# Optimization experiments

Hardware: AMD Instinct MI355X
Metric: run time of the kernel (lower is better)

## Reference

```python
import jax, jax.numpy as jnp
import numpy as np

L = 12; D = 768; H = 12; HD = 64; FF = 3072; P = 16; IMG = 224; BLK = 64
LORA = 16.0 / 64.0  # lora_alpha / r
PD = 512; B = 8


def _ln(x, g, b, eps=1e-6):
    m = x.mean(-1, keepdims=True)
    v = ((x - m) ** 2).mean(-1, keepdims=True)
    return (x - m) * jax.lax.rsqrt(v + eps) * g + b


def _dq(q, s):
    # int4 codes [O, I] + blockwise absmax-style scales [O, I//BLK] -> fp32 weight
    O, I = q.shape
    return ((q.astype(jnp.float32).reshape(O, I // BLK, BLK) - 7.5) * s[:, :, None]).reshape(O, I)


def _forward(img, patch_w, patch_b, cls_token, ln1_g, ln1_b, ln2_g, ln2_b, g1, g2,
             qkv_s, qkv_b, a_qkv, b_qkv, proj_s, proj_b, a_proj, b_proj,
             fc1_s, fc1_b, fc2_s, fc2_b, fcn_g, fcn_b, head_w, head_b,
             qkv_q, proj_q, fc1_q, fc2_q):
    x = img[:, 0]                                   # [B,3,224,224]
    Bn = x.shape[0]
    gp = IMG // P
    # patch embed (conv16x16/s16 == unfold + matmul)
    p = x.reshape(Bn, 3, gp, P, gp, P).transpose(0, 2, 4, 1, 3, 5).reshape(Bn, gp * gp, 3 * P * P)
    tok = p @ patch_w.T + patch_b                   # [B,196,768]
    cls = jnp.broadcast_to(cls_token, (Bn, 1, D))
    x = jnp.concatenate([cls, tok], axis=1)         # [B,197,768]

    def block(x, pr):
        (l1g, l1b, l2g, l2b, gm1, gm2, qq, qs, qb, aQ, bQ,
         pq, ps, pb, aP, bP, f1q, f1s, f1b, f2q, f2s, f2b) = pr
        h = _ln(x, l1g, l1b)
        # fused dequant + matmul + LoRA (qkv)
        qkv = h @ _dq(qq, qs).T + qb + LORA * ((h @ aQ.T) @ bQ.T)  # [B,N,3D]
        q, k, v = jnp.split(qkv, 3, axis=-1)
        heads = lambda t: t.reshape(Bn, -1, H, HD).transpose(0, 2, 1, 3)
        q, k, v = heads(q), heads(k), heads(v)
        attn = jax.nn.softmax(jnp.einsum('bhnd,bhmd->bhnm', q, k) / np.sqrt(HD).astype(np.float32), axis=-1)
        o = jnp.einsum('bhnm,bhmd->bhnd', attn, v).transpose(0, 2, 1, 3).reshape(Bn, -1, D)
        # dequant + matmul + LoRA (attn out proj)
        o = o @ _dq(pq, ps).T + pb + LORA * ((o @ aP.T) @ bP.T)
        x = x + gm1 * o                             # layerscale residual
        h = _ln(x, l2g, l2b)
        h = jax.nn.gelu(h @ _dq(f1q, f1s).T + f1b)
        h = h @ _dq(f2q, f2s).T + f2b
        x = x + gm2 * h
        return x, None

    xs = (ln1_g, ln1_b, ln2_g, ln2_b, g1, g2, qkv_q, qkv_s, qkv_b, a_qkv, b_qkv,
          proj_q, proj_s, proj_b, a_proj, b_proj, fc1_q, fc1_s, fc1_b, fc2_q, fc2_s, fc2_b)
    x, _ = jax.lax.scan(block, x, xs)
    pooled = x[:, 1:].mean(axis=1)                  # BEiT avg-pool over patch tokens
    pooled = _ln(pooled, fcn_g, fcn_b)              # fc_norm
    return jax.nn.relu(pooled @ head_w.T + head_b)  # Linear + ReLU projection -> [B,512]


def setup_inputs() -> dict:
    key = jax.random.key(0)
    ks = jax.random.split(key, 24)
    f = lambda i, sh, sc=0.02: jax.random.normal(ks[i], sh, dtype=jnp.float32) * sc
    u = lambda i, sh: jax.random.uniform(ks[i], sh, dtype=jnp.float32) * 0.01 + 1e-3
    qi = lambda i, sh: jax.random.randint(ks[i], sh, 0, 16, dtype=jnp.int32)
    return {
        'img': f(0, (B, 1, 3, IMG, IMG), 1.0),
        'patch_w': f(1, (D, 3 * P * P)), 'patch_b': jnp.zeros((D,), jnp.float32),
        'cls_token': f(2, (1, 1, D)),
        'ln1_g': jnp.ones((L, D), jnp.float32), 'ln1_b': jnp.zeros((L, D), jnp.float32),
        'ln2_g': jnp.ones((L, D), jnp.float32), 'ln2_b': jnp.zeros((L, D), jnp.float32),
        'g1': jnp.full((L, D), 0.1, jnp.float32), 'g2': jnp.full((L, D), 0.1, jnp.float32),
        'qkv_q': qi(3, (L, 3 * D, D)), 'qkv_s': u(4, (L, 3 * D, D // BLK)), 'qkv_b': f(5, (L, 3 * D)),
        'a_qkv': f(6, (L, 64, D)), 'b_qkv': f(7, (L, 3 * D, 64)),
        'proj_q': qi(8, (L, D, D)), 'proj_s': u(9, (L, D, D // BLK)), 'proj_b': jnp.zeros((L, D), jnp.float32),
        'a_proj': f(10, (L, 64, D)), 'b_proj': f(11, (L, D, 64)),
        'fc1_q': qi(12, (L, FF, D)), 'fc1_s': u(13, (L, FF, D // BLK)), 'fc1_b': jnp.zeros((L, FF), jnp.float32),
        'fc2_q': qi(14, (L, D, FF)), 'fc2_s': u(15, (L, D, FF // BLK)), 'fc2_b': jnp.zeros((L, D), jnp.float32),
        'fcn_g': jnp.ones((D,), jnp.float32), 'fcn_b': jnp.zeros((D,), jnp.float32),
        'head_w': f(16, (PD, D)), 'head_b': jnp.zeros((PD,), jnp.float32),
    }


def reference(img, patch_w, patch_b, cls_token, ln1_g, ln1_b, ln2_g, ln2_b, g1, g2,
              qkv_q, qkv_s, qkv_b, a_qkv, b_qkv, proj_q, proj_s, proj_b, a_proj, b_proj,
              fc1_q, fc1_s, fc1_b, fc2_q, fc2_s, fc2_b, fcn_g, fcn_b, head_w, head_b):
    return _forward(img, patch_w, patch_b, cls_token, ln1_g, ln1_b, ln2_g, ln2_b, g1, g2,
                    qkv_s, qkv_b, a_qkv, b_qkv, proj_s, proj_b, a_proj, b_proj,
                    fc1_s, fc1_b, fc2_s, fc2_b, fcn_g, fcn_b, head_w, head_b,
                    qkv_q, proj_q, fc1_q, fc2_q)
```

## Files before the change

kernel.cpp:

```cpp
#include <hip/hip_runtime.h>
#include <hip/hip_bf16.h>

using bf16 = __hip_bfloat16;
typedef __attribute__((ext_vector_type(8))) short short8;
typedef __attribute__((ext_vector_type(4))) float f32x4;
typedef __attribute__((ext_vector_type(4))) int i32x4;

#define NTOK 197
#define MTOK 1576
#define MPATCH 1568

static __device__ __forceinline__ float bf2f(bf16 v){ return __bfloat162float(v); }
static __device__ __forceinline__ bf16 f2bf(float v){ return __float2bfloat16(v); }
static __device__ __forceinline__ unsigned pk2(float a, float b){
  union{ bf16 h[2]; unsigned u; } r; r.h[0]=f2bf(a); r.h[1]=f2bf(b); return r.u;
}

static __device__ __forceinline__ float gelu_tanh(float x){
  float x3 = x*x*x;
  float a = 0.7978845608028654f*(x + 0.044715f*x3);
  float e = __expf(-2.f*fabsf(a));
  float t = (1.f-e)/(1.f+e);
  t = (a >= 0.f) ? t : -t;
  return 0.5f*x*(1.f+t);
}

static __device__ __forceinline__ void gload16(const void* g, void* l){
  __builtin_amdgcn_global_load_lds(
      (const __attribute__((address_space(1))) unsigned*)g,
      (__attribute__((address_space(3))) unsigned*)l, 16, 0, 0);
}

template<int N> static __device__ __forceinline__ void wait_vm(){
  if constexpr (N==3)      asm volatile("s_waitcnt vmcnt(3)" ::: "memory");
  else if constexpr (N==5) asm volatile("s_waitcnt vmcnt(5)" ::: "memory");
  else                     asm volatile("s_waitcnt vmcnt(0)" ::: "memory");
}

template<int K>
static __device__ __forceinline__ void dq16(const int* __restrict__ q,
                                            const float* __restrict__ s,
                                            bf16* __restrict__ o, int j){
  constexpr int KP16 = K/16;
  int n = j / KP16;
  int k = (j - n*KP16) * 16;
  const i32x4* qp = (const i32x4*)(q + (size_t)n*K + k);
  i32x4 a0 = __builtin_nontemporal_load(qp);
  i32x4 a1 = __builtin_nontemporal_load(qp + 1);
  i32x4 a2 = __builtin_nontemporal_load(qp + 2);
  i32x4 a3 = __builtin_nontemporal_load(qp + 3);
  float sc = s[(size_t)n*(K>>6) + (k>>6)];
  uint4 r0, r1;
  r0.x = pk2(((float)a0.x-7.5f)*sc, ((float)a0.y-7.5f)*sc);
  r0.y = pk2(((float)a0.z-7.5f)*sc, ((float)a0.w-7.5f)*sc);
  r0.z = pk2(((float)a1.x-7.5f)*sc, ((float)a1.y-7.5f)*sc);
  r0.w = pk2(((float)a1.z-7.5f)*sc, ((float)a1.w-7.5f)*sc);
  r1.x = pk2(((float)a2.x-7.5f)*sc, ((float)a2.y-7.5f)*sc);
  r1.y = pk2(((float)a2.z-7.5f)*sc, ((float)a2.w-7.5f)*sc);
  r1.z = pk2(((float)a3.x-7.5f)*sc, ((float)a3.y-7.5f)*sc);
  r1.w = pk2(((float)a3.z-7.5f)*sc, ((float)a3.w-7.5f)*sc);
  bf16* op = o + (size_t)n*K + k;
  *(uint4*)(op)     = r0;
  *(uint4*)(op + 8) = r1;
}

template<int K>
__global__ void dq_k(const int* __restrict__ q, const float* __restrict__ s,
                     bf16* __restrict__ o, int total16){
  #pragma unroll 2
  for (int j = blockIdx.x*256 + threadIdx.x; j < total16; j += gridDim.x*256)
    dq16<K>(q, s, o, j);
}

__global__ void cvtall_k(const float* __restrict__ patchw, bf16* __restrict__ patchwb,
                         const float* __restrict__ headw, bf16* __restrict__ headwb,
                         const float* __restrict__ bQ, bf16* __restrict__ bQs,
                         const float* __restrict__ bP, bf16* __restrict__ bPs){
  const int R0 = 768*768/4, R1 = R0 + 512*768/4;
  const int R2 = R1 + 12*2304*64/4, R3 = R2 + 12*768*64/4;
  for (int i = blockIdx.x*256 + threadIdx.x; i < R3; i += gridDim.x*256){
    const float* in; bf16* out; float a; int j;
    if (i < R0){ in=patchw; out=patchwb; a=1.f; j=i; }
    else if (i < R1){ in=headw; out=headwb; a=1.f; j=i-R0; }
    else if (i < R2){ in=bQ; out=bQs; a=0.25f; j=i-R1; }
    else { in=bP; out=bPs; a=0.25f; j=i-R2; }
    float4 v = *(const float4*)(in + (size_t)j*4);
    uint2 r; r.x = pk2(v.x*a, v.y*a); r.y = pk2(v.z*a, v.w*a);
    *(uint2*)(out + (size_t)j*4) = r;
  }
}

__global__ __launch_bounds__(256) void transall_k(const float* __restrict__ aQ, bf16* __restrict__ aQT,
                                                  const float* __restrict__ aP, bf16* __restrict__ aPT){
  __shared__ float tile[64][65];
  const float* in = blockIdx.z ? aP : aQ;
  bf16* out = blockIdx.z ? aPT : aQT;
  const int l = blockIdx.y, c0 = blockIdx.x*64;
  const int t = threadIdx.x;
  const int r = t >> 2, cq = (t & 3) * 16;
  const float* src = in + (size_t)l*64*768 + (size_t)r*768 + c0 + cq;
  #pragma unroll
  for (int j=0;j<4;j++){
    float4 v = *(const float4*)(src + j*4);
    tile[r][cq + j*4 + 0] = v.x; tile[r][cq + j*4 + 1] = v.y;
    tile[r][cq + j*4 + 2] = v.z; tile[r][cq + j*4 + 3] = v.w;
  }
  __syncthreads();
  unsigned w[8];
  #pragma unroll
  for (int j=0;j<8;j++)
    w[j] = pk2(tile[cq + 2*j][r], tile[cq + 2*j + 1][r]);
  bf16* dst = out + ((size_t)l*768 + c0 + r)*64 + cq;
  *(uint4*)(dst)     = *(uint4*)&w[0];
  *(uint4*)(dst + 8) = *(uint4*)&w[4];
}

__global__ void patchify_k(const float* __restrict__ img, bf16* __restrict__ p){
  int idx = blockIdx.x*256 + threadIdx.x;
  if (idx >= MPATCH*768) return;
  int col = idx % 768, pr = idx / 768;
  int b = pr / 196, patch = pr % 196;
  int c = col >> 8, rem = col & 255, py = rem >> 4, px = rem & 15;
  int gy = patch / 14, gx = patch % 14;
  float v = img[(((size_t)(b*3 + c))*224 + gy*16 + py)*224 + gx*16 + px];
  p[idx] = f2bf(v);
}

__global__ void cls_k(const float* __restrict__ cls, float* __restrict__ x){
  int i = blockIdx.x*256 + threadIdx.x;
  if (i >= 8*768) return;
  int b = i / 768, d = i % 768;
  x[(size_t)(b*NTOK)*768 + d] = cls[d];
}

__global__ __launch_bounds__(256) void ln_k(const float* __restrict__ x,
                                            const float* __restrict__ g,
                                            const float* __restrict__ b,
                                            bf16* __restrict__ out, int M){
  int row = blockIdx.x*4 + (threadIdx.x >> 6);
  int lane = threadIdx.x & 63;
  if (row >= M) return;
  const float* xr = x + (size_t)row*768;
  float4 v[3]; float s = 0.f;
  #pragma unroll
  for (int j=0;j<3;j++){
    v[j] = *(const float4*)(xr + lane*4 + j*256);
    s += v[j].x + v[j].y + v[j].z + v[j].w;
  }
  #pragma unroll
  for (int o=32;o;o>>=1) s += __shfl_xor(s, o);
  float mean = s * (1.f/768.f);
  float vs = 0.f;
  #pragma unroll
  for (int j=0;j<3;j++){
    float dx=v[j].x-mean, dy=v[j].y-mean, dz=v[j].z-mean, dw=v[j].w-mean;
    vs += dx*dx + dy*dy + dz*dz + dw*dw;
  }
  #pragma unroll
  for (int o=32;o;o>>=1) vs += __shfl_xor(vs, o);
  float rs = rsqrtf(vs*(1.f/768.f) + 1e-6f);
  bf16* orow = out + (size_t)row*768;
  #pragma unroll
  for (int j=0;j<3;j++){
    int d0 = lane*4 + j*256;
    float4 gv = *(const float4*)(g + d0);
    float4 bv = *(const float4*)(b + d0);
    uint2 pk;
    pk.x = pk2((v[j].x-mean)*rs*gv.x + bv.x, (v[j].y-mean)*rs*gv.y + bv.y);
    pk.y = pk2((v[j].z-mean)*rs*gv.z + bv.z, (v[j].w-mean)*rs*gv.w + bv.w);
    *(uint2*)(orow + d0) = pk;
  }
}

__global__ __launch_bounds__(256) void attn_k(const bf16* __restrict__ qkv, bf16* __restrict__ o){
  __shared__ char Kc[2][32*128];
  __shared__ bf16 Vt[2][64][40];
  __shared__ bf16 Pl[4][32][40];

  const int blk = blockIdx.x;
  const int half = blk & 1, bh = blk >> 1;
  const int b = bh / 12, h = bh % 12;
  const int t = threadIdx.x, wave = t>>6, lane = t&63;
  const int qbase = half*128 + wave*32;
  const bf16* base = qkv + (size_t)b*NTOK*2304 + h*64;

  short8 qf[2][2];
  #pragma unroll
  for (int qt=0;qt<2;qt++){
    int row = qbase + qt*16 + (lane&15); row = row < NTOK ? row : NTOK-1;
    const bf16* qr = base + (size_t)row*2304 + (lane>>4)*8;
    qf[qt][0] = *(const short8*)(qr);
    qf[qt][1] = *(const short8*)(qr + 32);
  }

  f32x4 Oa[2][4];
  float mrow[2][4], srow[2][4];
  #pragma unroll
  for (int i=0;i<2;i++)
    #pragma unroll
    for (int j=0;j<4;j++){ Oa[i][j] = (f32x4){0.f,0.f,0.f,0.f}; }
  #pragma unroll
  for (int i=0;i<2;i++)
    #pragma unroll
    for (int j=0;j<4;j++){ mrow[i][j] = -1e30f; srow[i][j] = 0.f; }

  const int sr = t>>3, sc = (t&7)*8;
  auto ldK = [&](int c)->uint4{
    int kv = c*32 + sr; kv = kv < NTOK ? kv : NTOK-1;
    return *(const uint4*)(base + (size_t)kv*2304 + 768 + sc);
  };
  auto ldV = [&](int c)->uint4{
    int kv = c*32 + sr;
    uint4 r = {0,0,0,0};
    if (kv < NTOK) r = *(const uint4*)(base + (size_t)kv*2304 + 1536 + sc);
    return r;
  };
  auto wrK = [&](int buf, uint4 kvv){
    *(uint4*)(Kc[buf] + sr*128 + ((sc*2) ^ ((sr&7)<<4))) = kvv;
  };
  auto wrV = [&](int buf, uint4 vvv){
    union{ uint4 u; short s[8]; } w; w.u = vvv;
    #pragma unroll
    for (int j=0;j<8;j++) *(short*)&Vt[buf][sc+j][sr] = w.s[j];
  };

  { uint4 k0 = ldK(0), v0 = ldV(0); wrK(0,k0); wrV(0,v0); }
  __syncthreads();

  for (int c=0;c<7;c++){
    const int buf = c & 1;
    uint4 kn, vn; const bool pf = (c < 6);
    if (pf){ kn = ldK(c+1); vn = ldV(c+1); }

    f32x4 S[2][2];
    #pragma unroll
    for (int i=0;i<2;i++)
      #pragma unroll
      for (int j=0;j<2;j++) S[i][j] = (f32x4){0.f,0.f,0.f,0.f};
    #pragma unroll
    for (int kt=0;kt<2;kt++){
      int rk = kt*16 + (lane&15);
      const char* kb = Kc[buf] + rk*128;
      int swz = (rk&7)<<4;
      short8 b0 = *(const short8*)(kb + (((lane>>4)*16) ^ swz));
      short8 b1 = *(const short8*)(kb + ((64 + (lane>>4)*16) ^ swz));
      #pragma unroll
      for (int qt=0;qt<2;qt++){
        S[qt][kt] = __builtin_amdgcn_mfma_f32_16x16x32_bf16(qf[qt][0], b0, S[qt][kt],0,0,0);
        S[qt][kt] = __builtin_amdgcn_mfma_f32_16x16x32_bf16(qf[qt][1], b1, S[qt][kt],0,0,0);
      }
    }

    #pragma unroll
    for (int qt=0;qt<2;qt++){
      #pragma unroll
      for (int r=0;r<4;r++){
        float s0 = S[qt][0][r]*0.125f, s1 = S[qt][1][r]*0.125f;
        if (c == 6){
          if (192 + (lane&15) >= NTOK) s0 = -1e30f;
          s1 = -1e30f;
        }
        float mx = fmaxf(s0, s1);
        mx = fmaxf(mx, __shfl_xor(mx,1));
        mx = fmaxf(mx, __shfl_xor(mx,2));
        mx = fmaxf(mx, __shfl_xor(mx,4));
        mx = fmaxf(mx, __shfl_xor(mx,8));
        float mo = mrow[qt][r];
        float mn = fmaxf(mo, mx);
        float scl = __expf(mo - mn);
        mrow[qt][r] = mn;
        float p0 = __expf(s0 - mn), p1 = __expf(s1 - mn);
        srow[qt][r] = srow[qt][r]*scl + p0 + p1;
        #pragma unroll
        for (int dt=0;dt<4;dt++) Oa[qt][dt][r] *= scl;
        int pr = qt*16 + (lane>>4)*4 + r;
        Pl[wave][pr][lane&15]      = f2bf(p0);
        Pl[wave][pr][16+(lane&15)] = f2bf(p1);
      }
    }

    short8 vb[4];
    #pragma unroll
    for (int dt=0;dt<4;dt++)
      vb[dt] = *(const short8*)(&Vt[buf][dt*16+(lane&15)][(lane>>4)*8]);
    #pragma unroll
    for (int qt=0;qt<2;qt++){
      short8 pa = *(const short8*)(&Pl[wave][qt*16+(lane&15)][(lane>>4)*8]);
      #pragma unroll
      for (int dt=0;dt<4;dt++)
        Oa[qt][dt] = __builtin_amdgcn_mfma_f32_16x16x32_bf16(pa, vb[dt], Oa[qt][dt],0,0,0);
    }

    if (pf){ wrK(buf^1, kn); wrV(buf^1, vn); }
    __syncthreads();
  }

  #pragma unroll
  for (int qt=0;qt<2;qt++)
    #pragma unroll
    for (int r=0;r<4;r++){
      float s = srow[qt][r];
      s += __shfl_xor(s,1); s += __shfl_xor(s,2);
      s += __shfl_xor(s,4); s += __shfl_xor(s,8);
      srow[qt][r] = 1.f/s;
    }
  #pragma unroll
  for (int qt=0;qt<2;qt++){
    #pragma unroll
    for (int r=0;r<4;r++){
      int tok = qbase + qt*16 + (lane>>4)*4 + r;
      if (tok < NTOK){
        bf16* orow = o + ((size_t)(b*NTOK+tok))*768 + h*64 + (lane&15);
        float inv = srow[qt][r];
        #pragma unroll
        for (int dt=0;dt<4;dt++) orow[dt*16] = f2bf(Oa[qt][dt][r]*inv);
      }
    }
  }
}

__global__ void pool_k(const float* __restrict__ x, float* __restrict__ pooled){
  int idx = blockIdx.x*256 + threadIdx.x;
  if (idx >= 8*768) return;
  int b = idx / 768, d = idx % 768;
  const float* col = x + (size_t)(b*NTOK)*768 + d;
  float s0=0.f, s1=0.f, s2=0.f, s3=0.f;
  for (int i=1; i<=196; i+=4){
    s0 += col[(size_t)i*768];
    s1 += col[(size_t)(i+1)*768];
    s2 += col[(size_t)(i+2)*768];
    s3 += col[(size_t)(i+3)*768];
  }
  pooled[idx] = (s0+s1+s2+s3) * (1.f/196.f);
}

template<int BM, int BN, int OUTMODE, int ACT, int FOLD>
__global__ __launch_bounds__(256) void gemm_k(
    const bf16* __restrict__ A, const bf16* __restrict__ W,
    const float* __restrict__ bias, const float* __restrict__ gvec,
    void* __restrict__ Cout,
    int M, int N, int Kst, int kiters, size_t kslab)
{
  constexpr int WCM = BM/2;
  constexpr int WCN = BN/2;
  constexpr int FM  = WCM/16;
  constexpr int FN  = WCN/16;
  constexpr int NW  = BN/32;
  constexpr int LCNT = 1 + NW;

  __shared__ char As[2][BM*128];
  __shared__ char Bs[2][BN*128];

  int mt, nt;
  {
    int gmy = gridDim.y;
    int nwg = gridDim.x * gmy;
    int bid = blockIdx.y * gridDim.x + blockIdx.x;
    int q8 = nwg >> 3, r8 = nwg & 7, xcd = bid & 7, idx = bid >> 3;
    int swz = (xcd < r8 ? xcd*(q8+1) : r8*(q8+1) + (xcd-r8)*q8) + idx;
    nt = swz / gmy; mt = swz - nt*gmy;
  }
  if (FOLD){
    A += (size_t)blockIdx.z * (size_t)M * 64;
    W += (size_t)blockIdx.z * (size_t)N * 64;
  }
  const int kz = FOLD ? 0 : blockIdx.z;
  const int k0 = kz * kiters;
  const int t = threadIdx.x, wave = t>>6, lane = t&63;
  const int wr = wave>>1, wc = wave&1;
  const int KT = kiters;

  const int srow = t >> 3;
  const int swzc = ((t&7)<<4) ^ ((srow&7)<<4);

  f32x4 acc[FM][FN];
  #pragma unroll
  for (int i=0;i<FM;i++)
    #pragma unroll
    for (int j=0;j<FN;j++) acc[i][j] = (f32x4){0.f,0.f,0.f,0.f};

  auto STAGE = [&](int it, int buf){
    {
      int gm = mt*BM + srow; gm = gm < M ? gm : M-1;
      gload16((const char*)A + (size_t)gm*Kst*2 + (size_t)(k0+it)*128 + swzc,
              As[buf] + wave*1024);
    }
    #pragma unroll
    for (int c=0;c<NW;c++){
      int gn = nt*BN + 32*c + srow;
      gload16((const char*)W + (size_t)gn*Kst*2 + (size_t)(k0+it)*128 + swzc,
              Bs[buf] + c*4096 + wave*1024);
    }
  };

  const int lrow = lane & 15;
  const int lkb  = (lane >> 4) * 16;
  auto computeTile = [&](int buf){
    __builtin_amdgcn_s_setprio(1);
    #pragma unroll
    for (int kk=0; kk<2; kk++){
      short8 af[FM]; short8 bw[FN];
      #pragma unroll
      for (int f=0; f<FM; f++){
        int ra = wr*WCM + f*16 + lrow;
        af[f] = *(const short8*)(As[buf] + ra*128 + ((kk*64 + lkb) ^ ((ra&7)<<4)));
      }
      #pragma unroll
      for (int f=0; f<FN; f++){
        int rb = wc*WCN + f*16 + lrow;
        bw[f] = *(const short8*)(Bs[buf] + rb*128 + ((kk*64 + lkb) ^ ((rb&7)<<4)));
      }
      #pragma unroll
      for (int i=0;i<FM;i++)
        #pragma unroll
        for (int j=0;j<FN;j++)
          acc[i][j] = __builtin_amdgcn_mfma_f32_16x16x32_bf16(af[i], bw[j], acc[i][j], 0, 0, 0);
    }
    __builtin_amdgcn_s_setprio(0);
  };

  STAGE(0, 0);
  if (KT > 1) STAGE(1, 1);

  for (int it = 0; it < KT; ++it){
    if (it == KT-1) wait_vm<0>(); else wait_vm<LCNT>();
    __builtin_amdgcn_s_barrier();
    computeTile(it & 1);
    asm volatile("s_waitcnt lgkmcnt(0)" ::: "memory");
    __builtin_amdgcn_s_barrier();
    if (it+2 < KT) STAGE(it+2, it & 1);
  }

  const int erow = (lane >> 4) * 4, ecol = lane & 15;
  #pragma unroll
  for (int i=0;i<FM;i++){
    #pragma unroll
    for (int j=0;j<FN;j++){
      int n = nt*BN + wc*WCN + j*16 + ecol;
      float bv = (bias != nullptr) ? bias[n] : 0.f;
      float gv = (OUTMODE==2) ? gvec[n] : 0.f;
      #pragma unroll
      for (int q=0; q<4; q++){
        int m = mt*BM + wr*WCM + i*16 + erow + q;
        if (m < M){
          float v = acc[i][j][q] + bv;
          if (ACT == 1) v = gelu_tanh(v);
          if (ACT == 2) v = fmaxf(v, 0.f);
          size_t off = (size_t)m*N + n;
          if (OUTMODE == 0)      ((float*)Cout)[(size_t)kz*kslab + off] = v;
          else if (OUTMODE == 1) ((bf16*)Cout)[off] = f2bf(v);
          else if (OUTMODE == 2) ((float*)Cout)[off] += gv * v;
          else if (OUTMODE == 4){
            int bb = m / 196, rr = m - bb*196;
            ((float*)Cout)[((size_t)(bb*NTOK + rr + 1))*768 + n] = v;
          }
          else {
            bf16* C = (bf16*)Cout + (FOLD ? (size_t)blockIdx.z*(size_t)M*N : (size_t)0);
            C[off] = f2bf(bf2f(C[off]) + v);
          }
        }
      }
    }
  }
}

extern "C" void kernel_launch(void* const* d_in, const int* in_sizes, int n_in,
                              void* d_out, int out_size, void* d_ws, size_t ws_size,
                              hipStream_t stream){
  (void)in_sizes; (void)n_in; (void)out_size; (void)ws_size;
  const float* img    = (const float*)d_in[0];
  const float* patchw = (const float*)d_in[1];
  const float* patchb = (const float*)d_in[2];
  const float* cls    = (const float*)d_in[3];
  const float* ln1g   = (const float*)d_in[4];
  const float* ln1b   = (const float*)d_in[5];
  const float* ln2g   = (const float*)d_in[6];
  const float* ln2b   = (const float*)d_in[7];
  const float* g1     = (const float*)d_in[8];
  const float* g2     = (const float*)d_in[9];
  const int*   qkvq   = (const int*)d_in[10];
  const float* qkvs   = (const float*)d_in[11];
  const float* qkvb   = (const float*)d_in[12];
  const float* aQ     = (const float*)d_in[13];
  const float* bQ     = (const float*)d_in[14];
  const int*   projq  = (const int*)d_in[15];
  const float* projs  = (const float*)d_in[16];
  const float* projb  = (const float*)d_in[17];
  const float* aP     = (const float*)d_in[18];
  const float* bP     = (const float*)d_in[19];
  const int*   fc1q   = (const int*)d_in[20];
  const float* fc1s   = (const float*)d_in[21];
  const float* fc1b   = (const float*)d_in[22];
  const int*   fc2q   = (const int*)d_in[23];
  const float* fc2s   = (const float*)d_in[24];
  const float* fc2b   = (const float*)d_in[25];
  const float* fcn_g  = (const float*)d_in[26];
  const float* fcn_b  = (const float*)d_in[27];
  const float* headw  = (const float*)d_in[28];
  const float* headb  = (const float*)d_in[29];
  float* out = (float*)d_out;

  char* wp = (char*)d_ws;
  auto alloc = [&](size_t bytes)->char* {
    char* r = wp; wp += (bytes + 255) & ~(size_t)255; return r;
  };
  float* x      = (float*)alloc((size_t)MTOK*768*4);
  bf16*  qkvo   = (bf16*) alloc((size_t)MTOK*2304*2);
  bf16*  h      = (bf16*) alloc((size_t)MTOK*768*2);
  bf16*  h1     = (bf16*) alloc((size_t)MTOK*3072*2);
  bf16*  ob     = (bf16*) alloc((size_t)MTOK*768*2);
  bf16*  p      = (bf16*) alloc((size_t)MPATCH*768*2);
  float* pooled = (float*)alloc((size_t)8*768*4);
  bf16*  pooledb= (bf16*) alloc((size_t)8*768*2);
  bf16* wqb = (bf16*)alloc((size_t)12*2304*768*2);
  bf16* wpb = (bf16*)alloc((size_t)12*768*768*2);
  bf16* w1b = (bf16*)alloc((size_t)12*3072*768*2);
  bf16* w2b = (bf16*)alloc((size_t)12*768*3072*2);
  bf16* patchwb = (bf16*)alloc((size_t)768*768*2);
  bf16* headwb  = (bf16*)alloc((size_t)512*768*2);
  bf16* bQs = (bf16*)alloc((size_t)12*2304*64*2);
  bf16* bPs = (bf16*)alloc((size_t)12*768*64*2);
  bf16* aQT = (bf16*)alloc((size_t)12*768*64*2);
  bf16* aPT = (bf16*)alloc((size_t)12*768*64*2);

  const int GM32 = (MTOK + 31) / 32;

  dq_k<768><<<2048, 256, 0, stream>>>(qkvq, qkvs, wqb, 12*2304*768/16);
  dq_k<768><<<2048, 256, 0, stream>>>(projq, projs, wpb, 12*768*768/16);
  dq_k<768><<<2048, 256, 0, stream>>>(fc1q, fc1s, w1b, 6*3072*768/16);
  dq_k<768><<<2048, 256, 0, stream>>>(fc1q + (size_t)6*3072*768, fc1s + (size_t)6*3072*12,
                                      w1b + (size_t)6*3072*768, 6*3072*768/16);
  dq_k<3072><<<2048, 256, 0, stream>>>(fc2q, fc2s, w2b, 6*768*3072/16);
  dq_k<3072><<<2048, 256, 0, stream>>>(fc2q + (size_t)6*768*3072, fc2s + (size_t)6*768*48,
                                       w2b + (size_t)6*768*3072, 6*768*3072/16);
  cvtall_k<<<1024, 256, 0, stream>>>(patchw, patchwb, headw, headwb, bQ, bQs, bP, bPs);
  transall_k<<<dim3(12, 12, 2), 256, 0, stream>>>(aQ, aQT, aP, aPT);
  gemm_k<32,64,3,0,1><<<dim3(768/64, 2304/32, 12), 256, 0, stream>>>(
      bQs, aQT, nullptr, nullptr, wqb, 2304, 768, 64, 1, 0);
  gemm_k<32,64,3,0,1><<<dim3(768/64, 768/32, 12), 256, 0, stream>>>(
      bPs, aPT, nullptr, nullptr, wpb, 768, 768, 64, 1, 0);

  patchify_k<<<(MPATCH*768 + 255)/256, 256, 0, stream>>>(img, p);
  gemm_k<32,64,4,0,0><<<dim3(768/64, MPATCH/32, 1), 256, 0, stream>>>(
      p, patchwb, patchb, nullptr, x, MPATCH, 768, 768, 12, 0);
  cls_k<<<(8*768 + 255)/256, 256, 0, stream>>>(cls, x);

  for (int l=0; l<12; l++){
    const bf16* wq_l = wqb + (size_t)l*2304*768;
    const bf16* wp_l = wpb + (size_t)l*768*768;
    const bf16* w1_l = w1b + (size_t)l*3072*768;
    const bf16* w2_l = w2b + (size_t)l*768*3072;

    ln_k<<<(MTOK+3)/4, 256, 0, stream>>>(x, ln1g + l*768, ln1b + l*768, h, MTOK);
    gemm_k<32,128,1,0,0><<<dim3(2304/128, GM32, 1), 256, 0, stream>>>(
        h, wq_l, qkvb + (size_t)l*2304, nullptr, qkvo, MTOK, 2304, 768, 12, 0);
    attn_k<<<192, 256, 0, stream>>>(qkvo, ob);
    gemm_k<32,64,2,0,0><<<dim3(768/64, GM32, 1), 256, 0, stream>>>(
        ob, wp_l, projb + (size_t)l*768, g1 + l*768, x, MTOK, 768, 768, 12, 0);

    ln_k<<<(MTOK+3)/4, 256, 0, stream>>>(x, ln2g + l*768, ln2b + l*768, h, MTOK);
    gemm_k<32,128,1,1,0><<<dim3(3072/128, GM32, 1), 256, 0, stream>>>(
        h, w1_l, fc1b + (size_t)l*3072, nullptr, h1, MTOK, 3072, 768, 12, 0);
    gemm_k<32,64,2,0,0><<<dim3(768/64, GM32, 1), 256, 0, stream>>>(
        h1, w2_l, fc2b + (size_t)l*768, g2 + l*768, x, MTOK, 768, 3072, 48, 0);
  }

  pool_k<<<(8*768 + 255)/256, 256, 0, stream>>>(x, pooled);
  ln_k<<<2, 256, 0, stream>>>(pooled, fcn_g, fcn_b, pooledb, 8);
  gemm_k<32,128,0,2,0><<<dim3(512/128, 1, 1), 256, 0, stream>>>(
      pooledb, headwb, headb, nullptr, out, 8, 512, 768, 12, 0);
}
```

Baseline: 1.473 ms.

## Split attention into 64-query blocks and fuse pooling, norm and head

The attention kernel now uses 128-thread blocks with 4 query groups per batch-head, giving 384 blocks instead of 192. Waves whose queries fall past the sequence end skip compute but still help load K/V tiles. Separately, mean pooling, final layernorm and the head linear+ReLU are fused into one tail kernel, replacing three launches. The variance in the tail kernel is now computed as E[x^2]-mean^2, which can lose precision compared with the two-pass form.

After: 1.541 ms. 1.05x slower.

```diff
diff --git a/kernel.cpp b/kernel.cpp
--- a/kernel.cpp
+++ b/kernel.cpp
@@ -12,6 +12,9 @@
 
 static __device__ __forceinline__ float bf2f(bf16 v){ return __bfloat162float(v); }
 static __device__ __forceinline__ bf16 f2bf(float v){ return __float2bfloat16(v); }
+static __device__ __forceinline__ float bfs(short s){
+  union{ unsigned u; float f; } c; c.u = ((unsigned)(unsigned short)s) << 16; return c.f;
+}
 static __device__ __forceinline__ unsigned pk2(float a, float b){
   union{ bf16 h[2]; unsigned u; } r; r.h[0]=f2bf(a); r.h[1]=f2bf(b); return r.u;
 }
@@ -172,25 +175,28 @@
   }
 }
 
-__global__ __launch_bounds__(256) void attn_k(const bf16* __restrict__ qkv, bf16* __restrict__ o){
+__global__ __launch_bounds__(128) void attn_k(const bf16* __restrict__ qkv, bf16* __restrict__ o){
   __shared__ char Kc[2][32*128];
   __shared__ bf16 Vt[2][64][40];
-  __shared__ bf16 Pl[4][32][40];
+  __shared__ bf16 Pl[2][32][40];
 
   const int blk = blockIdx.x;
-  const int half = blk & 1, bh = blk >> 1;
+  const int grp = blk & 3, bh = blk >> 2;
   const int b = bh / 12, h = bh % 12;
   const int t = threadIdx.x, wave = t>>6, lane = t&63;
-  const int qbase = half*128 + wave*32;
+  const int qbase = grp*64 + wave*32;
+  const bool alive = qbase < NTOK;
   const bf16* base = qkv + (size_t)b*NTOK*2304 + h*64;
 
   short8 qf[2][2];
-  #pragma unroll
-  for (int qt=0;qt<2;qt++){
-    int row = qbase + qt*16 + (lane&15); row = row < NTOK ? row : NTOK-1;
-    const bf16* qr = base + (size_t)row*2304 + (lane>>4)*8;
-    qf[qt][0] = *(const short8*)(qr);
-    qf[qt][1] = *(const short8*)(qr + 32);
+  if (alive){
+    #pragma unroll
+    for (int qt=0;qt<2;qt++){
+      int row = qbase + qt*16 + (lane&15); row = row < NTOK ? row : NTOK-1;
+      const bf16* qr = base + (size_t)row*2304 + (lane>>4)*8;
+      qf[qt][0] = *(const short8*)(qr);
+      qf[qt][1] = *(const short8*)(qr + 32);
+    }
   }
 
   f32x4 Oa[2][4];
@@ -198,140 +204,192 @@
   #pragma unroll
   for (int i=0;i<2;i++)
     #pragma unroll
-    for (int j=0;j<4;j++){ Oa[i][j] = (f32x4){0.f,0.f,0.f,0.f}; }
-  #pragma unroll
-  for (int i=0;i<2;i++)
-    #pragma unroll
-    for (int j=0;j<4;j++){ mrow[i][j] = -1e30f; srow[i][j] = 0.f; }
-
-  const int sr = t>>3, sc = (t&7)*8;
-  auto ldK = [&](int c)->uint4{
+    for (int j=0;j<4;j++){ Oa[i][j] = (f32x4){0.f,0.f,0.f,0.f}; mrow[i][j] = -1e30f; srow[i][j] = 0.f; }
+
+  const int sr = t>>2, scq = (t&3)*16;
+  auto ldK = [&](int c, uint4& k0, uint4& k1){
     int kv = c*32 + sr; kv = kv < NTOK ? kv : NTOK-1;
-    return *(const uint4*)(base + (size_t)kv*2304 + 768 + sc);
+    const bf16* kp = base + (size_t)kv*2304 + 768 + scq;
+    k0 = *(const uint4*)(kp);
+    k1 = *(const uint4*)(kp + 8);
   };
-  auto ldV = [&](int c)->uint4{
+  auto ldV = [&](int c, uint4& v0, uint4& v1){
     int kv = c*32 + sr;
-    uint4 r = {0,0,0,0};
-    if (kv < NTOK) r = *(const uint4*)(base + (size_t)kv*2304 + 1536 + sc);
-    return r;
+    v0 = (uint4){0,0,0,0}; v1 = (uint4){0,0,0,0};
+    if (kv < NTOK){
+      const bf16* vp = base + (size_t)kv*2304 + 1536 + scq;
+      v0 = *(const uint4*)(vp);
+      v1 = *(const uint4*)(vp + 8);
+    }
   };
-  auto wrK = [&](int buf, uint4 kvv){
-    *(uint4*)(Kc[buf] + sr*128 + ((sc*2) ^ ((sr&7)<<4))) = kvv;
+  auto wrK = [&](int buf, uint4 k0, uint4 k1){
+    int swz = (sr&7)<<4, cb = scq*2;
+    *(uint4*)(Kc[buf] + sr*128 + (cb ^ swz))        = k0;
+    *(uint4*)(Kc[buf] + sr*128 + ((cb+16) ^ swz))   = k1;
   };
-  auto wrV = [&](int buf, uint4 vvv){
-    union{ uint4 u; short s[8]; } w; w.u = vvv;
-    #pragma unroll
-    for (int j=0;j<8;j++) *(short*)&Vt[buf][sc+j][sr] = w.s[j];
+  auto wrV = [&](int buf, uint4 v0, uint4 v1){
+    union{ uint4 u; short s[8]; } w0, w1; w0.u = v0; w1.u = v1;
+    #pragma unroll
+    for (int j=0;j<8;j++){
+      *(short*)&Vt[buf][scq+j][sr]   = w0.s[j];
+      *(short*)&Vt[buf][scq+8+j][sr] = w1.s[j];
+    }
   };
 
-  { uint4 k0 = ldK(0), v0 = ldV(0); wrK(0,k0); wrV(0,v0); }
+  { uint4 k0,k1,v0,v1; ldK(0,k0,k1); ldV(0,v0,v1); wrK(0,k0,k1); wrV(0,v0,v1); }
   __syncthreads();
 
   for (int c=0;c<7;c++){
     const int buf = c & 1;
-    uint4 kn, vn; const bool pf = (c < 6);
-    if (pf){ kn = ldK(c+1); vn = ldV(c+1); }
-
-    f32x4 S[2][2];
-    #pragma unroll
-    for (int i=0;i<2;i++)
-      #pragma unroll
-      for (int j=0;j<2;j++) S[i][j] = (f32x4){0.f,0.f,0.f,0.f};
-    #pragma unroll
-    for (int kt=0;kt<2;kt++){
-      int rk = kt*16 + (lane&15);
-      const char* kb = Kc[buf] + rk*128;
-      int swz = (rk&7)<<4;
-      short8 b0 = *(const short8*)(kb + (((lane>>4)*16) ^ swz));
-      short8 b1 = *(const short8*)(kb + ((64 + (lane>>4)*16) ^ swz));
+    uint4 kn0,kn1,vn0,vn1; const bool pf = (c < 6);
+    if (pf){ ldK(c+1,kn0,kn1); ldV(c+1,vn0,vn1); }
+
+    if (alive){
+      f32x4 S[2][2];
+      #pragma unroll
+      for (int i=0;i<2;i++)
+        #pragma unroll
+        for (int j=0;j<2;j++) S[i][j] = (f32x4){0.f,0.f,0.f,0.f};
+      #pragma unroll
+      for (int kt=0;kt<2;kt++){
+        int rk = kt*16 + (lane&15);
+        const char* kb = Kc[buf] + rk*128;
+        int swz = (rk&7)<<4;
+        short8 b0 = *(const short8*)(kb + (((lane>>4)*16) ^ swz));
+        short8 b1 = *(const short8*)(kb + ((64 + (lane>>4)*16) ^ swz));
+        #pragma unroll
+        for (int qt=0;qt<2;qt++){
+          S[qt][kt] = __builtin_amdgcn_mfma_f32_16x16x32_bf16(qf[qt][0], b0, S[qt][kt],0,0,0);
+          S[qt][kt] = __builtin_amdgcn_mfma_f32_16x16x32_bf16(qf[qt][1], b1, S[qt][kt],0,0,0);
+        }
+      }
+
       #pragma unroll
       for (int qt=0;qt<2;qt++){
-        S[qt][kt] = __builtin_amdgcn_mfma_f32_16x16x32_bf16(qf[qt][0], b0, S[qt][kt],0,0,0);
-        S[qt][kt] = __builtin_amdgcn_mfma_f32_16x16x32_bf16(qf[qt][1], b1, S[qt][kt],0,0,0);
-      }
-    }
-
+        #pragma unroll
+        for (int r=0;r<4;r++){
+          float s0 = S[qt][0][r]*0.125f, s1 = S[qt][1][r]*0.125f;
+          if (c == 6){
+            if (192 + (lane&15) >= NTOK) s0 = -1e30f;
+            s1 = -1e30f;
+          }
+          float mx = fmaxf(s0, s1);
+          mx = fmaxf(mx, __shfl_xor(mx,1));
+          mx = fmaxf(mx, __shfl_xor(mx,2));
+          mx = fmaxf(mx, __shfl_xor(mx,4));
+          mx = fmaxf(mx, __shfl_xor(mx,8));
+          float mo = mrow[qt][r];
+          float mn = fmaxf(mo, mx);
+          float scl = __expf(mo - mn);
+          mrow[qt][r] = mn;
+          float p0 = __expf(s0 - mn), p1 = __expf(s1 - mn);
+          srow[qt][r] = srow[qt][r]*scl + p0 + p1;
+          #pragma unroll
+          for (int dt=0;dt<4;dt++) Oa[qt][dt][r] *= scl;
+          int pr = qt*16 + (lane>>4)*4 + r;
+          Pl[wave][pr][lane&15]      = f2bf(p0);
+          Pl[wave][pr][16+(lane&15)] = f2bf(p1);
+        }
+      }
+
+      short8 vb[4];
+      #pragma unroll
+      for (int dt=0;dt<4;dt++)
+        vb[dt] = *(const short8*)(&Vt[buf][dt*16+(lane&15)][(lane>>4)*8]);
+      #pragma unroll
+      for (int qt=0;qt<2;qt++){
+        short8 pa = *(const short8*)(&Pl[wave][qt*16+(lane&15)][(lane>>4)*8]);
+        #pragma unroll
+        for (int dt=0;dt<4;dt++)
+          Oa[qt][dt] = __builtin_amdgcn_mfma_f32_16x16x32_bf16(pa, vb[dt], Oa[qt][dt],0,0,0);
+      }
+    }
+
+    if (pf){ wrK(buf^1, kn0, kn1); wrV(buf^1, vn0, vn1); }
+    __syncthreads();
+  }
+
+  if (alive){
+    #pragma unroll
+    for (int qt=0;qt<2;qt++)
+      #pragma unroll
+      for (int r=0;r<4;r++){
+        float s = srow[qt][r];
+        s += __shfl_xor(s,1); s += __shfl_xor(s,2);
+        s += __shfl_xor(s,4); s += __shfl_xor(s,8);
+        srow[qt][r] = 1.f/s;
+      }
     #pragma unroll
     for (int qt=0;qt<2;qt++){
       #pragma unroll
       for (int r=0;r<4;r++){
-        float s0 = S[qt][0][r]*0.125f, s1 = S[qt][1][r]*0.125f;
-        if (c == 6){
-          if (192 + (lane&15) >= NTOK) s0 = -1e30f;
-          s1 = -1e30f;
+        int tok = qbase + qt*16 + (lane>>4)*4 + r;
+        if (tok < NTOK){
+          bf16* orow = o + ((size_t)(b*NTOK+tok))*768 + h*64 + (lane&15);
+          float inv = srow[qt][r];
+          #pragma unroll
+          for (int dt=0;dt<4;dt++) orow[dt*16] = f2bf(Oa[qt][dt][r]*inv);
         }
-        float mx = fmaxf(s0, s1);
-        mx = fmaxf(mx, __shfl_xor(mx,1));
-        mx = fmaxf(mx, __shfl_xor(mx,2));
-        mx = fmaxf(mx, __shfl_xor(mx,4));
-        mx = fmaxf(mx, __shfl_xor(mx,8));
-        float mo = mrow[qt][r];
-        float mn = fmaxf(mo, mx);
-        float scl = __expf(mo - mn);
-        mrow[qt][r] = mn;
-        float p0 = __expf(s0 - mn), p1 = __expf(s1 - mn);
-        srow[qt][r] = srow[qt][r]*scl + p0 + p1;
-        #pragma unroll
-        for (int dt=0;dt<4;dt++) Oa[qt][dt][r] *= scl;
-        int pr = qt*16 + (lane>>4)*4 + r;
-        Pl[wave][pr][lane&15]      = f2bf(p0);
-        Pl[wave][pr][16+(lane&15)] = f2bf(p1);
-      }
-    }
-
-    short8 vb[4];
-    #pragma unroll
-    for (int dt=0;dt<4;dt++)
-      vb[dt] = *(const short8*)(&Vt[buf][dt*16+(lane&15)][(lane>>4)*8]);
-    #pragma unroll
-    for (int qt=0;qt<2;qt++){
-      short8 pa = *(const short8*)(&Pl[wave][qt*16+(lane&15)][(lane>>4)*8]);
-      #pragma unroll
-      for (int dt=0;dt<4;dt++)
-        Oa[qt][dt] = __builtin_amdgcn_mfma_f32_16x16x32_bf16(pa, vb[dt], Oa[qt][dt],0,0,0);
-    }
-
-    if (pf){ wrK(buf^1, kn); wrV(buf^1, vn); }
-    __syncthreads();
-  }
-
-  #pragma unroll
-  for (int qt=0;qt<2;qt++)
-    #pragma unroll
-    for (int r=0;r<4;r++){
-      float s = srow[qt][r];
-      s += __shfl_xor(s,1); s += __shfl_xor(s,2);
-      s += __shfl_xor(s,4); s += __shfl_xor(s,8);
-      srow[qt][r] = 1.f/s;
-    }
-  #pragma unroll
-  for (int qt=0;qt<2;qt++){
-    #pragma unroll
-    for (int r=0;r<4;r++){
-      int tok = qbase + qt*16 + (lane>>4)*4 + r;
-      if (tok < NTOK){
-        bf16* orow = o + ((size_t)(b*NTOK+tok))*768 + h*64 + (lane&15);
-        float inv = srow[qt][r];
-        #pragma unroll
-        for (int dt=0;dt<4;dt++) orow[dt*16] = f2bf(Oa[qt][dt][r]*inv);
-      }
-    }
-  }
-}
-
-__global__ void pool_k(const float* __restrict__ x, float* __restrict__ pooled){
-  int idx = blockIdx.x*256 + threadIdx.x;
-  if (idx >= 8*768) return;
-  int b = idx / 768, d = idx % 768;
-  const float* col = x + (size_t)(b*NTOK)*768 + d;
-  float s0=0.f, s1=0.f, s2=0.f, s3=0.f;
-  for (int i=1; i<=196; i+=4){
-    s0 += col[(size_t)i*768];
-    s1 += col[(size_t)(i+1)*768];
-    s2 += col[(size_t)(i+2)*768];
-    s3 += col[(size_t)(i+3)*768];
-  }
-  pooled[idx] = (s0+s1+s2+s3) * (1.f/196.f);
+      }
+    }
+  }
+}
+
+__global__ __launch_bounds__(256) void tail_k(const float* __restrict__ x,
+                                              const float* __restrict__ fcng,
+                                              const float* __restrict__ fcnb,
+                                              const bf16* __restrict__ headwb,
+                                              const float* __restrict__ headb,
+                                              float* __restrict__ out){
+  __shared__ float pooled[768];
+  __shared__ bf16 nrm[768];
+  __shared__ float red[8];
+  const int b = blockIdx.x, t = threadIdx.x;
+  const int wave = t>>6, lane = t&63;
+  float acc[3];
+  #pragma unroll
+  for (int j=0;j<3;j++){
+    int d = t + j*256;
+    const float* col = x + (size_t)(b*NTOK)*768 + d;
+    float s0=0.f,s1=0.f,s2=0.f,s3=0.f;
+    for (int i=1;i<=196;i+=4){
+      s0 += col[(size_t)i*768];     s1 += col[(size_t)(i+1)*768];
+      s2 += col[(size_t)(i+2)*768]; s3 += col[(size_t)(i+3)*768];
+    }
+    acc[j] = (s0+s1+s2+s3) * (1.f/196.f);
+    pooled[d] = acc[j];
+  }
+  float ls=0.f, lq=0.f;
+  #pragma unroll
+  for (int j=0;j<3;j++){ ls += acc[j]; lq += acc[j]*acc[j]; }
+  #pragma unroll
+  for (int o=32;o;o>>=1){ ls += __shfl_xor(ls,o); lq += __shfl_xor(lq,o); }
+  if (lane==0){ red[wave] = ls; red[4+wave] = lq; }
+  __syncthreads();
+  float ts = red[0]+red[1]+red[2]+red[3];
+  float tq = red[4]+red[5]+red[6]+red[7];
+  float mean = ts * (1.f/768.f);
+  float var  = tq * (1.f/768.f) - mean*mean;
+  float rs = rsqrtf(var + 1e-6f);
+  #pragma unroll
+  for (int j=0;j<3;j++){
+    int d = t + j*256;
+    nrm[d] = f2bf((pooled[d]-mean)*rs*fcng[d] + fcnb[d]);
+  }
+  __syncthreads();
+  #pragma unroll
+  for (int j=0;j<2;j++){
+    int oo = t + j*256;
+    const bf16* wrow = headwb + (size_t)oo*768;
+    float a = 0.f;
+    for (int k=0;k<768;k+=8){
+      short8 wv = *(const short8*)(wrow + k);
+      short8 nv = *(const short8*)(&nrm[k]);
+      #pragma unroll
+      for (int e=0;e<8;e++) a += bfs(wv[e]) * bfs(nv[e]);
+    }
+    out[(size_t)b*512 + oo] = fmaxf(a + headb[oo], 0.f);
+  }
 }
 
 template<int BM, int BN, int OUTMODE, int ACT, int FOLD>
@@ -510,8 +568,6 @@
   bf16*  h1     = (bf16*) alloc((size_t)MTOK*3072*2);
   bf16*  ob     = (bf16*) alloc((size_t)MTOK*768*2);
   bf16*  p      = (bf16*) alloc((size_t)MPATCH*768*2);
-  float* pooled = (float*)alloc((size_t)8*768*4);
-  bf16*  pooledb= (bf16*) alloc((size_t)8*768*2);
   bf16* wqb = (bf16*)alloc((size_t)12*2304*768*2);
   bf16* wpb = (bf16*)alloc((size_t)12*768*768*2);
   bf16* w1b = (bf16*)alloc((size_t)12*3072*768*2);
@@ -554,7 +610,7 @@
     ln_k<<<(MTOK+3)/4, 256, 0, stream>>>(x, ln1g + l*768, ln1b + l*768, h, MTOK);
     gemm_k<32,128,1,0,0><<<dim3(2304/128, GM32, 1), 256, 0, stream>>>(
         h, wq_l, qkvb + (size_t)l*2304, nullptr, qkvo, MTOK, 2304, 768, 12, 0);
-    attn_k<<<192, 256, 0, stream>>>(qkvo, ob);
+    attn_k<<<384, 128, 0, stream>>>(qkvo, ob);
     gemm_k<32,64,2,0,0><<<dim3(768/64, GM32, 1), 256, 0, stream>>>(
         ob, wp_l, projb + (size_t)l*768, g1 + l*768, x, MTOK, 768, 768, 12, 0);
 
@@ -565,8 +621,5 @@
         h1, w2_l, fc2b + (size_t)l*768, g2 + l*768, x, MTOK, 768, 3072, 48, 0);
   }
 
-  pool_k<<<(8*768 + 255)/256, 256, 0, stream>>>(x, pooled);
-  ln_k<<<2, 256, 0, stream>>>(pooled, fcn_g, fcn_b, pooledb, 8);
-  gemm_k<32,128,0,2,0><<<dim3(512/128, 1, 1), 256, 0, stream>>>(
-      pooledb, headwb, headb, nullptr, out, 8, 512, 768, 12, 0);
-}
+  tail_k<<<8, 256, 0, stream>>>(x, fcn_g, fcn_b, headwb, headb, out);
+}
```
